# Kernel optimization log

Hardware: AMD Instinct MI355X
Metric: run time of the kernel (lower is better)

## Reference

```python
import jax, jax.numpy as jnp
import numpy as np

NUM_JOINTS = 33
EPS = 1e-5
# MediaPipe 33-landmark pose skeleton connections
SKELETON_EDGES = np.array([
    [0,1],[1,2],[2,3],[3,7],[0,4],[4,5],[5,6],[6,8],[9,10],
    [11,12],[11,13],[13,15],[15,17],[15,19],[15,21],[17,19],
    [12,14],[14,16],[16,18],[16,20],[16,22],[18,20],
    [11,23],[12,24],[23,24],[23,25],[24,26],[25,27],[26,28],
    [27,29],[28,30],[29,31],[30,32],[27,31],[28,32]], dtype=np.int64)


def _batched_edges(B):
    und = np.concatenate([SKELETON_EDGES, SKELETON_EDGES[:, ::-1]], axis=0)
    loops = np.stack([np.arange(NUM_JOINTS)] * 2, axis=1)
    e = np.concatenate([und, loops], axis=0)  # [103, 2] per graph (incl. self loops)
    eb = (e[None, :, :] + (np.arange(B) * NUM_JOINTS)[:, None, None]).reshape(-1, 2)
    return jnp.asarray(eb[:, 0], dtype=jnp.int32), jnp.asarray(eb[:, 1], dtype=jnp.int32)


def setup_inputs() -> dict:
    key = jax.random.key(0)
    B, N, F, H, L = 4096, NUM_JOINTS, 256, 256, 4
    ks = jax.random.split(key, 20)
    d = {"x": jax.random.normal(ks[0], (B, N, F), dtype=jnp.float32)}
    dims = [(F, H), (H, H), (H, H)]
    i = 1
    for li, (di, do) in enumerate(dims):
        d[f"w{li}"] = jax.random.normal(ks[i], (di, do), dtype=jnp.float32) * 0.05; i += 1
        d[f"b{li}"] = jnp.zeros((do,), dtype=jnp.float32)
        d[f"g{li}"] = jnp.ones((do,), dtype=jnp.float32)
        d[f"be{li}"] = jnp.zeros((do,), dtype=jnp.float32)
    d["wh"] = jax.random.normal(ks[i], (H, H), dtype=jnp.float32) * 0.05; i += 1
    d["bh"] = jnp.zeros((H,), dtype=jnp.float32)
    d["wc"] = jax.random.normal(ks[i], (H, L), dtype=jnp.float32) * 0.05; i += 1
    d["bc"] = jnp.zeros((L,), dtype=jnp.float32)
    src, dst = _batched_edges(B)
    d["src"], d["dst"] = src, dst
    return d


def _gcn_conv(x, W, b, src, dst, norm, num_nodes):
    h = x @ W                          # [NN, out]
    msg = h[src] * norm[:, None]       # gather + scale
    agg = jax.ops.segment_sum(msg, dst, num_segments=num_nodes)
    return agg + b


def _bn_relu(x, g, be):
    mu = jnp.mean(x, axis=0)
    var = jnp.mean((x - mu) ** 2, axis=0)  # biased, torch training BN
    return jax.nn.relu((x - mu) * jax.lax.rsqrt(var + EPS) * g + be)


def reference(x, w0, b0, g0, be0, w1, b1, g1, be1, w2, b2, g2, be2, wh, bh, wc, bc, src, dst):
    B, N, F = x.shape
    NN = B * N
    h = jnp.nan_to_num(x.reshape(NN, F))
    # symmetric GCN normalization D^{-1/2}(A+I)D^{-1/2}; self loops already in edge list
    deg = jax.ops.segment_sum(jnp.ones_like(src, dtype=h.dtype), dst, num_segments=NN)
    dinv = jax.lax.rsqrt(deg)
    norm = dinv[src] * dinv[dst]
    for W, b, g, be in ((w0, b0, g0, be0), (w1, b1, g1, be1), (w2, b2, g2, be2)):
        h = _gcn_conv(h, W, b, src, dst, norm, NN)
        h = _bn_relu(h, g, be)  # dropout: eval mode -> identity
    h = _gcn_conv(h, wh, bh, src, dst, norm, NN)
    pooled = h.reshape(B, N, -1).mean(axis=1)  # global mean pool per graph
    return pooled @ wc + bc
```

## Files before the change

### kernel.cpp

```cpp
#include <hip/hip_runtime.h>

typedef unsigned short u16;
typedef __attribute__((ext_vector_type(8))) short short8;
typedef __attribute__((ext_vector_type(4))) float floatx4;

#define NN_TOT 135168

static constexpr int NBCNT[33] = {2,2,2,2,2,2,2,1,1,1,1,3,3,2,2,4,4,2,2,2,2,1,1,3,3,2,2,3,3,2,2,2,2};
static constexpr int NBR[33][4] = {
 {1,4,0,0},{0,2,0,0},{1,3,0,0},{2,7,0,0},{0,5,0,0},{4,6,0,0},{5,8,0,0},
 {3,0,0,0},{6,0,0,0},{10,0,0,0},{9,0,0,0},
 {12,13,23,0},{11,14,24,0},{11,15,0,0},{12,16,0,0},
 {13,17,19,21},{14,18,20,22},
 {15,19,0,0},{16,20,0,0},{15,17,0,0},{16,18,0,0},{15,0,0,0},{16,0,0,0},
 {11,24,25,0},{12,23,26,0},{23,27,0,0},{24,28,0,0},
 {25,29,31,0},{26,30,32,0},{27,31,0,0},{28,32,0,0},{29,27,0,0},{30,28,0,0}};
static constexpr float R2 = 0.70710678f, R3 = 0.57735027f, R4 = 0.5f, R5 = 0.44721360f;
static constexpr float DINV[33] = {R3,R3,R3,R3,R3,R3,R3, R2,R2,R2,R2, R4,R4, R3,R3, R5,R5,
                                   R3,R3,R3,R3, R2,R2, R4,R4, R3,R3, R4,R4, R3,R3,R3,R3};

__device__ __forceinline__ float bf2f(u16 u) {
  unsigned int v = ((unsigned int)u) << 16; float f; __builtin_memcpy(&f, &v, 4); return f;
}
__device__ __forceinline__ u16 f2bf(float f) {
  unsigned int u; __builtin_memcpy(&u, &f, 4);
  return (u16)((u + 0x7fffu + ((u >> 16) & 1u)) >> 16);
}
__device__ __forceinline__ float ldin(const void* p, int i, int isbf) {
  return isbf ? bf2f(((const u16*)p)[i]) : ((const float*)p)[i];
}
__device__ __forceinline__ void gload_lds16(const u16* g, u16* l) {
  __builtin_amdgcn_global_load_lds((const __attribute__((address_space(1))) unsigned int*)g,
                                   (__attribute__((address_space(3))) unsigned int*)l, 16, 0, 0);
}

__global__ __launch_bounds__(256) void detect_kernel(const u16* __restrict__ x,
                                                     int* __restrict__ flag)
{
  __shared__ int cnt[256];
  const int t = threadIdx.x;
  int c = 0;
  for (int j = 0; j < 16; ++j) {
    u16 u = x[(t*16 + j)*2];
    int e = (u >> 7) & 0xFF;
    c += (e >= 118 && e <= 130) ? 1 : 0;
  }
  cnt[t] = c;
  __syncthreads();
  if (t == 0) {
    int s = 0;
    for (int i = 0; i < 256; ++i) s += cnt[i];
    *flag = (s > 2048) ? 1 : 0;
  }
}

__global__ __launch_bounds__(256) void transpose_kernel(const void* __restrict__ w0,
    const void* __restrict__ w1, const void* __restrict__ w2, u16* __restrict__ Wt,
    const int* __restrict__ flag)
{
  const int m = blockIdx.x >> 4;
  const int nb = (blockIdx.x & 15) * 16;
  const void* W = m == 0 ? w0 : (m == 1 ? w1 : w2);
  u16* O = Wt + (size_t)m * 65536;
  const int t = threadIdx.x;
  const int lane = t & 63, wv = t >> 6;
  const int isbf = *flag;
  if (isbf) {
    const u16* Wb = (const u16*)W;
#pragma unroll
    for (int nn = 0; nn < 4; ++nn) {
      const int n = nb + nn*4 + wv;
#pragma unroll
      for (int j = 0; j < 4; ++j) {
        const int k = lane + 64*j;
        O[n*256 + k] = Wb[k*256 + n];
      }
    }
  } else {
    const float* Wf = (const float*)W;
#pragma unroll
    for (int nn = 0; nn < 4; ++nn) {
      const int n = nb + nn*4 + wv;
#pragma unroll
      for (int j = 0; j < 4; ++j) {
        const int k = lane + 64*j;
        O[n*256 + k] = f2bf(Wf[k*256 + n]);
      }
    }
  }
}

__global__ __launch_bounds__(256) void init_kernel(const void* __restrict__ wh,
    const void* __restrict__ bh, const void* __restrict__ wc, const void* __restrict__ bc,
    float* __restrict__ wq, float* __restrict__ bq, float* __restrict__ repl,
    const int* __restrict__ flag)
{
  const int idx = blockIdx.x*256 + threadIdx.x;
  for (int i = idx; i < 3*64*512; i += 65*256) repl[i] = 0.f;
  const int isbf = *flag;
  const int t = threadIdx.x;
  const int lane = t & 63;
  if (blockIdx.x < 64) {
    const int r = blockIdx.x*4 + (t >> 6);
    float a0=0.f, a1=0.f, a2=0.f, a3=0.f;
#pragma unroll
    for (int j = 0; j < 4; ++j) {
      const int k = lane + 64*j;
      const float w = ldin(wh, r*256 + k, isbf);
      a0 += w*ldin(wc, k*4+0, isbf); a1 += w*ldin(wc, k*4+1, isbf);
      a2 += w*ldin(wc, k*4+2, isbf); a3 += w*ldin(wc, k*4+3, isbf);
    }
#pragma unroll
    for (int off = 32; off; off >>= 1) {
      a0 += __shfl_xor(a0, off); a1 += __shfl_xor(a1, off);
      a2 += __shfl_xor(a2, off); a3 += __shfl_xor(a3, off);
    }
    if (lane == 0) { wq[r*4+0]=a0; wq[r*4+1]=a1; wq[r*4+2]=a2; wq[r*4+3]=a3; }
  } else if (t < 64) {
    float s0=0.f, s1=0.f, s2=0.f, s3=0.f;
#pragma unroll
    for (int j = 0; j < 4; ++j) {
      const int k = lane + 64*j;
      const float b = ldin(bh, k, isbf);
      s0 += b*ldin(wc, k*4+0, isbf); s1 += b*ldin(wc, k*4+1, isbf);
      s2 += b*ldin(wc, k*4+2, isbf); s3 += b*ldin(wc, k*4+3, isbf);
    }
#pragma unroll
    for (int off = 32; off; off >>= 1) {
      s0 += __shfl_xor(s0, off); s1 += __shfl_xor(s1, off);
      s2 += __shfl_xor(s2, off); s3 += __shfl_xor(s3, off);
    }
    if (lane == 0) {
      bq[0] = s0 + ldin(bc, 0, isbf); bq[1] = s1 + ldin(bc, 1, isbf);
      bq[2] = s2 + ldin(bc, 2, isbf); bq[3] = s3 + ldin(bc, 3, isbf);
    }
  }
}

template<int ACT>
__global__ __launch_bounds__(256, 2) void fused_kernel(
    const void* __restrict__ Ag, const u16* __restrict__ Bt,
    const float* __restrict__ fscale, const float* __restrict__ fshift,
    const void* __restrict__ bias, u16* __restrict__ H,
    float* __restrict__ repl, const int* __restrict__ flag)
{
  __shared__ __align__(16) u16 smem[17424];
  u16* const sA = smem;
  u16* const sB = smem + 3072;
  const int tid = threadIdx.x;
  const int lane = tid & 63, w = tid >> 6;
  const int gi = w >> 1, h = w & 1;
  const int fr = lane & 15, q = lane >> 4;
  const size_t R0 = (size_t)blockIdx.x * 66;
  const int dtf = *flag;
  const int isbf = (ACT == 0) ? dtf : 1;

  const u16* Ab = (const u16*)Ag;
  const float* Af = (const float*)Ag;

  floatx4 acc[3][8];
#pragma unroll
  for (int t = 0; t < 3; ++t)
#pragma unroll
    for (int j = 0; j < 8; ++j) acc[t][j] = (floatx4){0.f, 0.f, 0.f, 0.f};

  const int r0 = tid >> 2;
  const int c8 = (tid & 3) * 8;
  const int lr = lane >> 2;
  const int lc = (lane & 3) * 8;

  for (int kc = 0; kc < 8; ++kc) {
    const int k0 = kc * 32;
    __syncthreads();
    if (ACT == 0 && isbf) {
      gload_lds16(Ab + (R0 + w*16 + lr)*256 + k0 + lc, sA + (w*16)*32);
      if (w == 0) {
        size_t rg = R0 + 64 + lr;
        if (rg >= NN_TOT) rg = NN_TOT - 1;
        if (lane < 8)
          gload_lds16(Ab + rg*256 + k0 + lc, sA + 64*32);
      }
    } else if (ACT == 0) {
      {
        const float* ap = Af + (R0 + r0)*256 + k0 + c8;
        float4 p0 = *(const float4*)(ap);
        float4 p1 = *(const float4*)(ap + 4);
        u16 ov[8];
        ov[0]=f2bf(p0.x); ov[1]=f2bf(p0.y); ov[2]=f2bf(p0.z); ov[3]=f2bf(p0.w);
        ov[4]=f2bf(p1.x); ov[5]=f2bf(p1.y); ov[6]=f2bf(p1.z); ov[7]=f2bf(p1.w);
        *(uint4*)(sA + r0*32 + c8) = *(const uint4*)ov;
      }
      if (tid < 8) {
        const int r = 64 + (tid >> 2);
        const float* ap = Af + (R0 + r)*256 + k0 + c8;
        float4 p0 = *(const float4*)(ap);
        float4 p1 = *(const float4*)(ap + 4);
        u16 ov[8];
        ov[0]=f2bf(p0.x); ov[1]=f2bf(p0.y); ov[2]=f2bf(p0.z); ov[3]=f2bf(p0.w);
        ov[4]=f2bf(p1.x); ov[5]=f2bf(p1.y); ov[6]=f2bf(p1.z); ov[7]=f2bf(p1.w);
        *(uint4*)(sA + r*32 + c8) = *(const uint4*)ov;
      }
    } else {
      float scv[8], shv[8];
#pragma unroll
      for (int j = 0; j < 8; ++j) { scv[j] = fscale[k0 + c8 + j]; shv[j] = fshift[k0 + c8 + j]; }
      {
        uint4 pk = *(const uint4*)(Ab + (R0 + r0)*256 + k0 + c8);
        const u16* us = (const u16*)&pk;
        u16 ov[8];
#pragma unroll
        for (int j = 0; j < 8; ++j) {
          float f = bf2f(us[j]);
          f = fmaxf(0.f, fmaf(f, scv[j], shv[j]));
          ov[j] = f2bf(f);
        }
        *(uint4*)(sA + r0*32 + c8) = *(const uint4*)ov;
      }
      if (tid < 8) {
        const int r = 64 + (tid >> 2);
        uint4 pk = *(const uint4*)(Ab + (R0 + r)*256 + k0 + c8);
        const u16* us = (const u16*)&pk;
        u16 ov[8];
#pragma unroll
        for (int j = 0; j < 8; ++j) {
          float f = bf2f(us[j]);
          f = fmaxf(0.f, fmaf(f, scv[j], shv[j]));
          ov[j] = f2bf(f);
        }
        *(uint4*)(sA + r*32 + c8) = *(const uint4*)ov;
      }
    }
#pragma unroll
    for (int i = 0; i < 4; ++i)
      gload_lds16(Bt + (w*64 + i*16 + lr)*256 + k0 + lc,
                  sB + (w*64 + i*16)*32);
    __syncthreads();

    short8 a[3], b[8];
#pragma unroll
    for (int t = 0; t < 3; ++t)
      a[t] = *(const short8*)(sA + (gi*33 + t*16 + fr)*32 + q*8);
#pragma unroll
    for (int nf = 0; nf < 8; ++nf)
      b[nf] = *(const short8*)(sB + (h*128 + nf*16 + fr)*32 + q*8);
#pragma unroll
    for (int t = 0; t < 3; ++t)
#pragma unroll
      for (int nf = 0; nf < 8; ++nf)
        acc[t][nf] = __builtin_amdgcn_mfma_f32_16x16x32_bf16(a[t], b[nf], acc[t][nf], 0, 0, 0);
  }

  __syncthreads();
  u16* const Tl = smem;
#pragma unroll
  for (int t = 0; t < 3; ++t)
#pragma unroll
    for (int nf = 0; nf < 8; ++nf)
#pragma unroll
      for (int r = 0; r < 4; ++r) {
        const int row = t*16 + q*4 + r;
        if (row < 33)
          Tl[(gi*33 + row)*264 + h*128 + nf*16 + fr] = f2bf(acc[t][nf][r]);
      }
  __syncthreads();

  const int g2 = tid >> 7, cp = tid & 127;
  const size_t Gg = (size_t)blockIdx.x*2 + g2;
  float a0[33], a1[33];
#pragma unroll
  for (int d = 0; d < 33; ++d) { a0[d] = 0.f; a1[d] = 0.f; }
#pragma unroll
  for (int s = 0; s < 33; ++s) {
    const unsigned int pk = *(const unsigned int*)(Tl + (g2*33 + s)*264 + cp*2);
    const float v0 = bf2f((u16)(pk & 0xffffu)) * DINV[s];
    const float v1 = bf2f((u16)(pk >> 16)) * DINV[s];
    a0[s] += v0; a1[s] += v1;
#pragma unroll
    for (int i = 0; i < NBCNT[s]; ++i) { a0[NBR[s][i]] += v0; a1[NBR[s][i]] += v1; }
  }
  const float bv0 = ldin(bias, cp*2,     dtf);
  const float bv1 = ldin(bias, cp*2 + 1, dtf);
  float s10 = 0.f, s20 = 0.f, s11 = 0.f, s21 = 0.f;
  u16* hg = H + Gg * (33*256);
#pragma unroll
  for (int d = 0; d < 33; ++d) {
    const float o0 = fmaf(a0[d], DINV[d], bv0);
    const float o1 = fmaf(a1[d], DINV[d], bv1);
    const unsigned int pw = (unsigned int)f2bf(o0) | ((unsigned int)f2bf(o1) << 16);
    *(unsigned int*)(hg + d*256 + cp*2) = pw;
    s10 += o0; s20 += o0*o0; s11 += o1; s21 += o1*o1;
  }
  float* r1p = repl + (Gg & 63)*512;
  atomicAdd(r1p + cp*2,           s10);
  atomicAdd(r1p + cp*2 + 1,       s11);
  atomicAdd(r1p + 256 + cp*2,     s20);
  atomicAdd(r1p + 256 + cp*2 + 1, s21);
}

__global__ __launch_bounds__(256) void statfin_kernel(const float* __restrict__ repl,
    const void* __restrict__ gamma, const void* __restrict__ beta, float* __restrict__ fs,
    const int* __restrict__ flag)
{
  const int c = threadIdx.x;
  const int isbf = *flag;
  float s1 = 0.f, s2 = 0.f;
  for (int r = 0; r < 64; ++r) { s1 += repl[r*512 + c]; s2 += repl[r*512 + 256 + c]; }
  const float inv = 1.f / (float)NN_TOT;
  const float mu = s1 * inv;
  const float var = s2 * inv - mu*mu;
  const float rs = rsqrtf(var + 1e-5f);
  const float sc = rs * ldin(gamma, c, isbf);
  fs[c] = sc;
  fs[256 + c] = ldin(beta, c, isbf) - mu * sc;
}

__global__ __launch_bounds__(256) void final_kernel(const u16* __restrict__ H,
    const float* __restrict__ fs, const float* __restrict__ wq,
    const float* __restrict__ bq, void* __restrict__ outp,
    const int* __restrict__ flag)
{
  const int g = blockIdx.x, c = threadIdx.x;
  const int isbf = *flag;
  const float sc = fs[c], sh = fs[256 + c];
  const u16* hg = H + (size_t)g * (33*256);
  float v = 0.f;
#pragma unroll
  for (int s = 0; s < 33; ++s) {
    float a = DINV[s];
#pragma unroll
    for (int i = 0; i < NBCNT[s]; ++i) a += DINV[NBR[s][i]];
    const float w = DINV[s] * a * (1.f/33.f);
    float x = bf2f(hg[s*256 + c]);
    x = fmaxf(0.f, fmaf(x, sc, sh));
    v += w * x;
  }
  float p0 = v*wq[c*4+0], p1 = v*wq[c*4+1], p2 = v*wq[c*4+2], p3 = v*wq[c*4+3];
#pragma unroll
  for (int off = 32; off; off >>= 1) {
    p0 += __shfl_xor(p0, off);
    p1 += __shfl_xor(p1, off);
    p2 += __shfl_xor(p2, off);
    p3 += __shfl_xor(p3, off);
  }
  __shared__ float sred[4][4];
  const int lane = c & 63, wid = c >> 6;
  if (lane == 0) { sred[wid][0]=p0; sred[wid][1]=p1; sred[wid][2]=p2; sred[wid][3]=p3; }
  __syncthreads();
  if (c < 4) {
    float r = sred[0][c] + sred[1][c] + sred[2][c] + sred[3][c] + bq[c];
    if (isbf) ((u16*)outp)[(size_t)g*4 + c] = f2bf(r);
    else      ((float*)outp)[(size_t)g*4 + c] = r;
  }
}

extern "C" void kernel_launch(void* const* d_in, const int* in_sizes, int n_in,
                              void* d_out, int out_size, void* d_ws, size_t ws_size,
                              hipStream_t stream)
{
  const void* x   = d_in[0];
  const void* w0  = d_in[1];
  const void* b0  = d_in[2];
  const void* g0  = d_in[3];
  const void* be0 = d_in[4];
  const void* w1  = d_in[5];
  const void* b1  = d_in[6];
  const void* g1  = d_in[7];
  const void* be1 = d_in[8];
  const void* w2  = d_in[9];
  const void* b2  = d_in[10];
  const void* g2  = d_in[11];
  const void* be2 = d_in[12];
  const void* wh  = d_in[13];
  const void* bh  = d_in[14];
  const void* wc  = d_in[15];
  const void* bc  = d_in[16];

  char* ws = (char*)d_ws;
  float* wq   = (float*)(ws + 0);
  float* bq   = (float*)(ws + 4096);
  float* fs   = (float*)(ws + 4608);
  int*   flag = (int*)  (ws + 12288);
  float* repl = (float*)(ws + 16384);
  u16*   Wt   = (u16*)  (ws + 409600);
  u16*   A    = (u16*)  (ws + 802816);
  (void)in_sizes; (void)n_in; (void)out_size; (void)ws_size;

  detect_kernel<<<1, 256, 0, stream>>>((const u16*)x, flag);
  transpose_kernel<<<48, 256, 0, stream>>>(w0, w1, w2, Wt, flag);
  init_kernel<<<65, 256, 0, stream>>>(wh, bh, wc, bc, wq, bq, repl, flag);

  fused_kernel<0><<<2048, 256, 0, stream>>>(x, Wt, nullptr, nullptr, b0, A, repl, flag);
  statfin_kernel<<<1, 256, 0, stream>>>(repl, g0, be0, fs, flag);
  fused_kernel<1><<<2048, 256, 0, stream>>>(A, Wt + 65536, fs, fs + 256, b1, A, repl + 32768, flag);
  statfin_kernel<<<1, 256, 0, stream>>>(repl + 32768, g1, be1, fs + 512, flag);
  fused_kernel<1><<<2048, 256, 0, stream>>>(A, Wt + 131072, fs + 512, fs + 768, b2, A, repl + 65536, flag);
  statfin_kernel<<<1, 256, 0, stream>>>(repl + 65536, g2, be2, fs + 1024, flag);
  final_kernel<<<4096, 256, 0, stream>>>(A, fs + 1024, wq, bq, d_out, flag);
}
```

Measured before the change: 448.3 us.

## Double-buffer LDS tiles with async prefetch and XOR-swizzled layout in fused GEMM

```diff
diff --git a/kernel.cpp b/kernel.cpp
--- a/kernel.cpp
+++ b/kernel.cpp
@@ -5,6 +5,9 @@
 typedef __attribute__((ext_vector_type(4))) float floatx4;
 
 #define NN_TOT 135168
+
+#define WAITVM(N) asm volatile("s_waitcnt vmcnt(" #N ")" ::: "memory")
+#define WAITLGKM0 asm volatile("s_waitcnt lgkmcnt(0)" ::: "memory")
 
 static constexpr int NBCNT[33] = {2,2,2,2,2,2,2,1,1,1,1,3,3,2,2,4,4,2,2,2,2,1,1,3,3,2,2,3,3,2,2,2,2};
 static constexpr int NBR[33][4] = {
@@ -33,6 +36,9 @@
   __builtin_amdgcn_global_load_lds((const __attribute__((address_space(1))) unsigned int*)g,
                                    (__attribute__((address_space(3))) unsigned int*)l, 16, 0, 0);
 }
+__device__ __forceinline__ int lof(int row, int qq) {
+  return row*32 + ((qq ^ ((row >> 1) & 3)) * 8);
+}
 
 __global__ __launch_bounds__(256) void detect_kernel(const u16* __restrict__ x,
                                                      int* __restrict__ flag)
@@ -144,13 +150,19 @@
     const void* __restrict__ bias, u16* __restrict__ H,
     float* __restrict__ repl, const int* __restrict__ flag)
 {
-  __shared__ __align__(16) u16 smem[17424];
-  u16* const sA = smem;
-  u16* const sB = smem + 3072;
+  __shared__ __align__(16) u16 smem[22528];
+  u16* const sA0 = smem;
+  u16* const sA1 = smem + 3072;
+  u16* const sB0 = smem + 6144;
+  u16* const sB1 = smem + 14336;
   const int tid = threadIdx.x;
   const int lane = tid & 63, w = tid >> 6;
   const int gi = w >> 1, h = w & 1;
   const int fr = lane & 15, q = lane >> 4;
+  const int lr = lane >> 2, cq = lane & 3;
+  const int swz = (lr >> 1) & 3;
+  const int r0 = tid >> 2;
+  const int c8 = (tid & 3) * 8;
   const size_t R0 = (size_t)blockIdx.x * 66;
   const int dtf = *flag;
   const int isbf = (ACT == 0) ? dtf : 1;
@@ -164,23 +176,81 @@
 #pragma unroll
     for (int j = 0; j < 8; ++j) acc[t][j] = (floatx4){0.f, 0.f, 0.f, 0.f};
 
-  const int r0 = tid >> 2;
-  const int c8 = (tid & 3) * 8;
-  const int lr = lane >> 2;
-  const int lc = (lane & 3) * 8;
-
-  for (int kc = 0; kc < 8; ++kc) {
-    const int k0 = kc * 32;
-    __syncthreads();
-    if (ACT == 0 && isbf) {
-      gload_lds16(Ab + (R0 + w*16 + lr)*256 + k0 + lc, sA + (w*16)*32);
-      if (w == 0) {
-        size_t rg = R0 + 64 + lr;
-        if (rg >= NN_TOT) rg = NN_TOT - 1;
-        if (lane < 8)
-          gload_lds16(Ab + rg*256 + k0 + lc, sA + 64*32);
-      }
-    } else if (ACT == 0) {
+  auto issueB = [&](u16* dst, int k0) {
+#pragma unroll
+    for (int i = 0; i < 4; ++i)
+      gload_lds16(Bt + (w*64 + i*16 + lr)*256 + k0 + (cq ^ swz)*8,
+                  dst + (w*64 + i*16)*32);
+  };
+  auto issueA_dma = [&](u16* dst, int k0) {
+    gload_lds16(Ab + (R0 + w*16 + lr)*256 + k0 + (cq ^ swz)*8, dst + (w*16)*32);
+    if (w == 0) {
+      size_t rg = R0 + 64 + lr;
+      if (rg >= NN_TOT) rg = NN_TOT - 1;
+      gload_lds16(Ab + rg*256 + k0 + (cq ^ swz)*8, dst + 64*32);
+    }
+  };
+
+  uint4 regA, regA2;
+  float sc8[8], sh8[8];
+  auto issueA_reg = [&](int k0) {
+    float4 t0 = *(const float4*)(fscale + k0 + c8);
+    float4 t1 = *(const float4*)(fscale + k0 + c8 + 4);
+    float4 t2 = *(const float4*)(fshift + k0 + c8);
+    float4 t3 = *(const float4*)(fshift + k0 + c8 + 4);
+    sc8[0]=t0.x; sc8[1]=t0.y; sc8[2]=t0.z; sc8[3]=t0.w;
+    sc8[4]=t1.x; sc8[5]=t1.y; sc8[6]=t1.z; sc8[7]=t1.w;
+    sh8[0]=t2.x; sh8[1]=t2.y; sh8[2]=t2.z; sh8[3]=t2.w;
+    sh8[4]=t3.x; sh8[5]=t3.y; sh8[6]=t3.z; sh8[7]=t3.w;
+    regA = *(const uint4*)(Ab + (R0 + r0)*256 + k0 + c8);
+    if (tid >= 248)
+      regA2 = *(const uint4*)(Ab + (R0 + 64 + ((tid - 248) >> 2))*256 + k0 + c8);
+  };
+  auto writeA = [&](u16* dst) {
+    {
+      const u16* us = (const u16*)&regA;
+      u16 ov[8];
+#pragma unroll
+      for (int j = 0; j < 8; ++j) {
+        float f = bf2f(us[j]);
+        f = fmaxf(0.f, fmaf(f, sc8[j], sh8[j]));
+        ov[j] = f2bf(f);
+      }
+      *(uint4*)(dst + r0*32 + ((cq ^ ((r0 >> 1) & 3))*8)) = *(const uint4*)ov;
+    }
+    if (tid >= 248) {
+      const int rr = 64 + ((tid - 248) >> 2);
+      const u16* us = (const u16*)&regA2;
+      u16 ov[8];
+#pragma unroll
+      for (int j = 0; j < 8; ++j) {
+        float f = bf2f(us[j]);
+        f = fmaxf(0.f, fmaf(f, sc8[j], sh8[j]));
+        ov[j] = f2bf(f);
+      }
+      *(uint4*)(dst + rr*32 + ((cq ^ ((rr >> 1) & 3))*8)) = *(const uint4*)ov;
+    }
+  };
+
+  auto compute = [&](const u16* cA, const u16* cB) {
+    short8 a[3], b[8];
+#pragma unroll
+    for (int t = 0; t < 3; ++t)
+      a[t] = *(const short8*)(cA + lof(gi*33 + t*16 + fr, q));
+#pragma unroll
+    for (int nf = 0; nf < 8; ++nf)
+      b[nf] = *(const short8*)(cB + lof(h*128 + nf*16 + fr, q));
+#pragma unroll
+    for (int t = 0; t < 3; ++t)
+#pragma unroll
+      for (int nf = 0; nf < 8; ++nf)
+        acc[t][nf] = __builtin_amdgcn_mfma_f32_16x16x32_bf16(a[t], b[nf], acc[t][nf], 0, 0, 0);
+  };
+
+  if (ACT == 0 && !isbf) {
+    for (int kc = 0; kc < 8; ++kc) {
+      const int k0 = kc * 32;
+      __syncthreads();
       {
         const float* ap = Af + (R0 + r0)*256 + k0 + c8;
         float4 p0 = *(const float4*)(ap);
@@ -188,66 +258,49 @@
         u16 ov[8];
         ov[0]=f2bf(p0.x); ov[1]=f2bf(p0.y); ov[2]=f2bf(p0.z); ov[3]=f2bf(p0.w);
         ov[4]=f2bf(p1.x); ov[5]=f2bf(p1.y); ov[6]=f2bf(p1.z); ov[7]=f2bf(p1.w);
-        *(uint4*)(sA + r0*32 + c8) = *(const uint4*)ov;
+        *(uint4*)(sA0 + r0*32 + ((cq ^ ((r0 >> 1) & 3))*8)) = *(const uint4*)ov;
       }
       if (tid < 8) {
-        const int r = 64 + (tid >> 2);
-        const float* ap = Af + (R0 + r)*256 + k0 + c8;
+        const int rr = 64 + (tid >> 2);
+        const float* ap = Af + (R0 + rr)*256 + k0 + c8;
         float4 p0 = *(const float4*)(ap);
         float4 p1 = *(const float4*)(ap + 4);
         u16 ov[8];
         ov[0]=f2bf(p0.x); ov[1]=f2bf(p0.y); ov[2]=f2bf(p0.z); ov[3]=f2bf(p0.w);
         ov[4]=f2bf(p1.x); ov[5]=f2bf(p1.y); ov[6]=f2bf(p1.z); ov[7]=f2bf(p1.w);
-        *(uint4*)(sA + r*32 + c8) = *(const uint4*)ov;
-      }
-    } else {
-      float scv[8], shv[8];
-#pragma unroll
-      for (int j = 0; j < 8; ++j) { scv[j] = fscale[k0 + c8 + j]; shv[j] = fshift[k0 + c8 + j]; }
-      {
-        uint4 pk = *(const uint4*)(Ab + (R0 + r0)*256 + k0 + c8);
-        const u16* us = (const u16*)&pk;
-        u16 ov[8];
-#pragma unroll
-        for (int j = 0; j < 8; ++j) {
-          float f = bf2f(us[j]);
-          f = fmaxf(0.f, fmaf(f, scv[j], shv[j]));
-          ov[j] = f2bf(f);
-        }
-        *(uint4*)(sA + r0*32 + c8) = *(const uint4*)ov;
-      }
-      if (tid < 8) {
-        const int r = 64 + (tid >> 2);
-        uint4 pk = *(const uint4*)(Ab + (R0 + r)*256 + k0 + c8);
-        const u16* us = (const u16*)&pk;
-        u16 ov[8];
-#pragma unroll
-        for (int j = 0; j < 8; ++j) {
-          float f = bf2f(us[j]);
-          f = fmaxf(0.f, fmaf(f, scv[j], shv[j]));
-          ov[j] = f2bf(f);
-        }
-        *(uint4*)(sA + r*32 + c8) = *(const uint4*)ov;
-      }
-    }
-#pragma unroll
-    for (int i = 0; i < 4; ++i)
-      gload_lds16(Bt + (w*64 + i*16 + lr)*256 + k0 + lc,
-                  sB + (w*64 + i*16)*32);
-    __syncthreads();
-
-    short8 a[3], b[8];
-#pragma unroll
-    for (int t = 0; t < 3; ++t)
-      a[t] = *(const short8*)(sA + (gi*33 + t*16 + fr)*32 + q*8);
-#pragma unroll
-    for (int nf = 0; nf < 8; ++nf)
-      b[nf] = *(const short8*)(sB + (h*128 + nf*16 + fr)*32 + q*8);
-#pragma unroll
-    for (int t = 0; t < 3; ++t)
-#pragma unroll
-      for (int nf = 0; nf < 8; ++nf)
-        acc[t][nf] = __builtin_amdgcn_mfma_f32_16x16x32_bf16(a[t], b[nf], acc[t][nf], 0, 0, 0);
+        *(uint4*)(sA0 + rr*32 + ((cq ^ ((rr >> 1) & 3))*8)) = *(const uint4*)ov;
+      }
+      issueB(sB0, k0);
+      __syncthreads();
+      compute(sA0, sB0);
+    }
+  } else {
+    if (ACT == 0) issueA_dma(sA0, 0); else issueA_reg(0);
+    issueB(sB0, 0);
+    if (ACT == 1) { WAITVM(4); writeA(sA0); WAITLGKM0; }
+
+    for (int kc = 0; kc < 8; ++kc) {
+      u16* curA = (kc & 1) ? sA1 : sA0;
+      u16* nxtA = (kc & 1) ? sA0 : sA1;
+      u16* curB = (kc & 1) ? sB1 : sB0;
+      u16* nxtB = (kc & 1) ? sB0 : sB1;
+      if (kc < 7) {
+        if (ACT == 0) issueA_dma(nxtA, (kc + 1) * 32);
+        else          issueA_reg((kc + 1) * 32);
+        issueB(nxtB, (kc + 1) * 32);
+      }
+      if (kc < 7) {
+        if (ACT == 0) { if (w == 0) { WAITVM(6); } else { WAITVM(5); } }
+        else          { if (w == 3) { WAITVM(10); } else { WAITVM(9); } }
+      } else { WAITVM(0); }
+      __builtin_amdgcn_sched_barrier(0);
+      __builtin_amdgcn_s_barrier();
+
+      compute(curA, curB);
+
+      if (ACT == 1 && kc < 7) { WAITVM(4); writeA(nxtA); }
+      WAITLGKM0;
+    }
   }
 
   __syncthreads();
```

New measurement: 423.0 us. -5.6%, faster.
